# Kernel tuning notes

Hardware: AMD Instinct MI355X
Metric: run time of the kernel (lower is better)

The kernel has to match this reference:

```python
import jax, jax.numpy as jnp
import numpy as np

B, T, D_IN, P, Q, D_OUT = 128, 1024, 64, 128, 2, 64


def _lstm_layer(x, w_ih, w_hh, b):
    """One LSTM layer, batch_first. x: [B,T,Din], w_ih: [4P,Din], w_hh: [4P,P], b: [4P].
    PyTorch gate order: i, f, g, o."""
    # Precompute input contribution for all timesteps (the big, parallel GEMM).
    gx = jnp.einsum('btd,gd->btg', x, w_ih) + b          # [B,T,4P]
    gx_t = jnp.swapaxes(gx, 0, 1)                        # [T,B,4P] for scan
    p = w_hh.shape[1]
    h0 = jnp.zeros((x.shape[0], p), dtype=x.dtype)
    c0 = jnp.zeros((x.shape[0], p), dtype=x.dtype)

    def step(carry, g_in):
        h, c = carry
        g = g_in + h @ w_hh.T                            # [B,4P]
        i, f, gg, o = jnp.split(g, 4, axis=-1)
        i = jax.nn.sigmoid(i)
        f = jax.nn.sigmoid(f)
        gg = jnp.tanh(gg)
        o = jax.nn.sigmoid(o)
        c = f * c + i * gg
        h = o * jnp.tanh(c)
        return (h, c), h

    _, hs = jax.lax.scan(step, (h0, c0), gx_t)           # hs: [T,B,P]
    return jnp.swapaxes(hs, 0, 1)                        # [B,T,P]


def setup_inputs() -> dict:
    key = jax.random.key(0)
    ks = jax.random.split(key, 8)
    x = jax.random.normal(ks[0], (B, T, D_IN), dtype=jnp.float32)
    # weight_ih: kaiming-normal-ish; weight_hh: orthogonal-ish (random normal is a fine stand-in
    # numerically; init distribution doesn't change the math being tested).
    w_ih0 = jax.random.normal(ks[1], (4 * P, D_IN), dtype=jnp.float32) * (1.0 / np.sqrt(D_IN))
    w_hh0 = jax.random.normal(ks[2], (4 * P, P), dtype=jnp.float32) * (1.0 / np.sqrt(P))
    w_ih1 = jax.random.normal(ks[3], (4 * P, P), dtype=jnp.float32) * (1.0 / np.sqrt(P))
    w_hh1 = jax.random.normal(ks[4], (4 * P, P), dtype=jnp.float32) * (1.0 / np.sqrt(P))
    # biases initialized to zero in the original (bias_ih + bias_hh folded into one per layer
    # would be equivalent math; keep both for faithfulness)
    b_ih = jnp.zeros((Q, 4 * P), dtype=jnp.float32)
    b_hh = jnp.zeros((Q, 4 * P), dtype=jnp.float32)
    fc_w = jax.random.normal(ks[5], (D_OUT, P), dtype=jnp.float32) * np.sqrt(2.0 / P)
    fc_b = jnp.zeros((D_OUT,), dtype=jnp.float32)
    return {"x": x, "w_ih0": w_ih0, "w_hh0": w_hh0, "w_ih1": w_ih1, "w_hh1": w_hh1,
            "b_ih": b_ih, "b_hh": b_hh, "fc_w": fc_w, "fc_b": fc_b}


def reference(x, w_ih0, w_hh0, w_ih1, w_hh1, b_ih, b_hh, fc_w, fc_b):
    h = _lstm_layer(x, w_ih0, w_hh0, b_ih[0] + b_hh[0])   # layer 0: [B,T,P]
    h = _lstm_layer(h, w_ih1, w_hh1, b_ih[1] + b_hh[1])   # layer 1: [B,T,P]
    return jnp.einsum('btp,op->bto', h, fc_w) + fc_b      # [B,T,D_OUT]
```

## Files before the change

### kernel.cpp

```cpp
#include <hip/hip_runtime.h>

#define NT 1024
#define RINGS 256

typedef _Float16 half8 __attribute__((ext_vector_type(8)));
typedef _Float16 half4 __attribute__((ext_vector_type(4)));
typedef float f32x4 __attribute__((ext_vector_type(4)));
typedef unsigned long long u64;
struct U2 { u64 a, b; };

__device__ __forceinline__ f32x4 MFMA(half8 a, half8 b, f32x4 c) {
  return __builtin_amdgcn_mfma_f32_16x16x32_f16(a, b, c, 0, 0, 0);
}
__device__ __forceinline__ float sigf(float x) {
  return __builtin_amdgcn_rcpf(1.0f + __expf(-x));
}
__device__ __forceinline__ float tanhf2(float x) {
  float ax = fabsf(x);
  float e = __expf(-2.0f * ax);
  float t = (1.0f - e) * __builtin_amdgcn_rcpf(1.0f + e);
  return copysignf(t, x);
}
__device__ __forceinline__ half8 cvt8(float4 c0, float4 c1) {
  half8 hv;
  hv[0] = (_Float16)c0.x; hv[1] = (_Float16)c0.y;
  hv[2] = (_Float16)c0.z; hv[3] = (_Float16)c0.w;
  hv[4] = (_Float16)c1.x; hv[5] = (_Float16)c1.y;
  hv[6] = (_Float16)c1.z; hv[7] = (_Float16)c1.w;
  return hv;
}
__device__ __forceinline__ half8 ldring(const _Float16* p) {
  const u64* q = (const u64*)p;
  U2 uu;
  uu.a = __hip_atomic_load(q, __ATOMIC_RELAXED, __HIP_MEMORY_SCOPE_AGENT);
  uu.b = __hip_atomic_load(q + 1, __ATOMIC_RELAXED, __HIP_MEMORY_SCOPE_AGENT);
  return __builtin_bit_cast(half8, uu);
}
__device__ __forceinline__ unsigned wpoll(unsigned* p, unsigned tgt,
                                          unsigned cached, int l) {
  unsigned c = cached;
  while (c < tgt) {
    unsigned pv = 0;
    if (l == 0)
      pv = __hip_atomic_load(p, __ATOMIC_ACQUIRE, __HIP_MEMORY_SCOPE_AGENT);
    c = (unsigned)__builtin_amdgcn_readfirstlane((int)pv);
    if (c < tgt) __builtin_amdgcn_s_sleep(2);
  }
  return c;
}

__global__ __launch_bounds__(256) void prep_x(const float* __restrict__ x,
                                              _Float16* __restrict__ Xf) {
  int t0 = blockIdx.x * 256 + threadIdx.x;
  int l = t0 & 63;
  int fid = t0 >> 6;
  int kt = fid & 1;
  int t = (fid >> 1) & (NT - 1);
  int g = fid >> 11;
  int bt = g * 16 + (l & 15);
  int kb = kt * 32 + (l >> 4) * 4;
  const float* src = x + ((size_t)bt * NT + (size_t)t) * 64 + kb;
  float4 v0 = *(const float4*)src;
  float4 v1 = *(const float4*)(src + 16);
  *(half8*)(Xf + (size_t)fid * 512 + l * 8) = cvt8(v0, v1);
}

__global__ __launch_bounds__(512, 1) void lstm_main(
    const float* __restrict__ wih0, const float* __restrict__ whh0,
    const float* __restrict__ wih1, const float* __restrict__ whh1,
    const float* __restrict__ bih, const float* __restrict__ bhh,
    const float* __restrict__ fcw, const float* __restrict__ fcb,
    const _Float16* __restrict__ Xf, _Float16* __restrict__ ringH0,
    unsigned* __restrict__ flags, float* __restrict__ out) {
  const int tid = threadIdx.x;
  const int w = tid >> 6, l = tid & 63;
  const int n = l & 15, lg = l >> 4;
  const bool producer = blockIdx.x < 8;
  const int g = blockIdx.x & 7;

  __shared__ _Float16 hfr[2][4][64][8];
  __shared__ _Float16 fcl[4][4][64][8];

  _Float16* ringG = ringH0 + (size_t)g * RINGS * 2048;
  unsigned* prog = flags + g * 16;
  unsigned* cons = flags + (8 + g) * 16;
  const half8 hz = {0, 0, 0, 0, 0, 0, 0, 0};

  if (producer) {
    half8 A[4][6];
    f32x4 bias[4];
#pragma unroll
    for (int q = 0; q < 4; ++q) {
      int row = (w + 8 * q) * 16 + n;
#pragma unroll
      for (int kt = 0; kt < 2; ++kt) {
        const float* wp = wih0 + (size_t)row * 64 + kt * 32 + lg * 4;
        A[q][kt] = cvt8(*(const float4*)wp, *(const float4*)(wp + 16));
      }
#pragma unroll
      for (int kt = 0; kt < 4; ++kt) {
        const float* wp = whh0 + (size_t)row * 128 + kt * 32 + lg * 4;
        A[q][2 + kt] = cvt8(*(const float4*)wp, *(const float4*)(wp + 16));
      }
      int rb = (w + 8 * q) * 16 + lg * 4;
      f32x4 bv;
#pragma unroll
      for (int r = 0; r < 4; ++r) bv[r] = bih[rb + r] + bhh[rb + r];
      bias[q] = bv;
    }
    if (tid < 256) ((half8*)&hfr[1][0][0][0])[tid] = hz;
    const _Float16* XfG = Xf + (size_t)g * NT * 1024;
    half8 x0 = *(const half8*)(XfG + l * 8);
    half8 x1 = *(const half8*)(XfG + 512 + l * 8);
    f32x4 cst = {0.f, 0.f, 0.f, 0.f};
    unsigned Cc = 0;
    __syncthreads();
    for (int s = 0; s < NT; ++s) {
      half8 xn0, xn1;
      if (s + 1 < NT) {
        const _Float16* p = XfG + (size_t)(s + 1) * 1024 + l * 8;
        xn0 = *(const half8*)p;
        xn1 = *(const half8*)(p + 512);
      }
      if (s >= 224 && (s & 31) == 0)
        Cc = wpoll(cons, (unsigned)(s - 192), Cc, l);
      const int rdk = (s + 1) & 1;
      half8 b2 = *(const half8*)&hfr[rdk][0][l][0];
      half8 b3 = *(const half8*)&hfr[rdk][1][l][0];
      half8 b4 = *(const half8*)&hfr[rdk][2][l][0];
      half8 b5 = *(const half8*)&hfr[rdk][3][l][0];
      f32x4 acc0 = bias[0], acc1 = bias[1], acc2 = bias[2], acc3 = bias[3];
      acc0 = MFMA(A[0][0], x0, acc0); acc1 = MFMA(A[1][0], x0, acc1);
      acc2 = MFMA(A[2][0], x0, acc2); acc3 = MFMA(A[3][0], x0, acc3);
      acc0 = MFMA(A[0][1], x1, acc0); acc1 = MFMA(A[1][1], x1, acc1);
      acc2 = MFMA(A[2][1], x1, acc2); acc3 = MFMA(A[3][1], x1, acc3);
      acc0 = MFMA(A[0][2], b2, acc0); acc1 = MFMA(A[1][2], b2, acc1);
      acc2 = MFMA(A[2][2], b2, acc2); acc3 = MFMA(A[3][2], b2, acc3);
      acc0 = MFMA(A[0][3], b3, acc0); acc1 = MFMA(A[1][3], b3, acc1);
      acc2 = MFMA(A[2][3], b3, acc2); acc3 = MFMA(A[3][3], b3, acc3);
      acc0 = MFMA(A[0][4], b4, acc0); acc1 = MFMA(A[1][4], b4, acc1);
      acc2 = MFMA(A[2][4], b4, acc2); acc3 = MFMA(A[3][4], b4, acc3);
      acc0 = MFMA(A[0][5], b5, acc0); acc1 = MFMA(A[1][5], b5, acc1);
      acc2 = MFMA(A[2][5], b5, acc2); acc3 = MFMA(A[3][5], b5, acc3);
      half4 hh;
#pragma unroll
      for (int r = 0; r < 4; ++r) {
        float iv = sigf(acc0[r]), fv = sigf(acc1[r]);
        float gv = tanhf2(acc2[r]), ov = sigf(acc3[r]);
        cst[r] = fv * cst[r] + iv * gv;
        hh[r] = (_Float16)(ov * tanhf2(cst[r]));
      }
      *(half4*)&hfr[s & 1][w >> 1][l][(w & 1) << 2] = hh;
      {
        u64 uh = __builtin_bit_cast(u64, hh);
        __hip_atomic_store(
            (u64*)(ringG + (size_t)(s & (RINGS - 1)) * 2048 +
                   (w >> 1) * 512 + l * 8 + (w & 1) * 4),
            uh, __ATOMIC_RELAXED, __HIP_MEMORY_SCOPE_AGENT);
      }
      asm volatile("s_waitcnt lgkmcnt(0)" ::: "memory");
      __builtin_amdgcn_sched_barrier(0);
      __builtin_amdgcn_s_barrier();
      __builtin_amdgcn_sched_barrier(0);
      if ((s & 31) == 31) {
        asm volatile("s_waitcnt vmcnt(0)" ::: "memory");
        __builtin_amdgcn_sched_barrier(0);
        __builtin_amdgcn_s_barrier();
        __builtin_amdgcn_sched_barrier(0);
        if (tid == 0)
          __hip_atomic_store(prog, (unsigned)(s + 1), __ATOMIC_RELEASE,
                             __HIP_MEMORY_SCOPE_AGENT);
      }
      x0 = xn0;
      x1 = xn1;
    }
  } else {
    half8 A[4][8];
    f32x4 bias[4], fcbv = {0.f, 0.f, 0.f, 0.f};
#pragma unroll
    for (int q = 0; q < 4; ++q) {
      int row = (w + 8 * q) * 16 + n;
#pragma unroll
      for (int kt = 0; kt < 4; ++kt) {
        const float* wp = wih1 + (size_t)row * 128 + kt * 32 + lg * 4;
        A[q][kt] = cvt8(*(const float4*)wp, *(const float4*)(wp + 16));
      }
#pragma unroll
      for (int kt = 0; kt < 4; ++kt) {
        const float* wp = whh1 + (size_t)row * 128 + kt * 32 + lg * 4;
        A[q][4 + kt] = cvt8(*(const float4*)wp, *(const float4*)(wp + 16));
      }
      int rb = (w + 8 * q) * 16 + lg * 4;
      f32x4 bv;
#pragma unroll
      for (int r = 0; r < 4; ++r)
        bv[r] = bih[512 + rb + r] + bhh[512 + rb + r];
      bias[q] = bv;
    }
    if (w < 4) {
      int frow = (w << 4) + n;
#pragma unroll
      for (int kt = 0; kt < 4; ++kt) {
        const float* wp = fcw + (size_t)frow * 128 + kt * 32 + lg * 4;
        *(half8*)&fcl[w][kt][l][0] =
            cvt8(*(const float4*)wp, *(const float4*)(wp + 16));
      }
      fcbv = *(const f32x4*)(fcb + (w << 4) + lg * 4);
    }
    if (tid < 256) ((half8*)&hfr[1][0][0][0])[tid] = hz;
    float* outG = out + (size_t)((g << 4) + n) * NT * 64 + (w << 4) + lg * 4;
    f32x4 cst = {0.f, 0.f, 0.f, 0.f};
    __syncthreads();
    unsigned Pc = wpoll(prog, 2u, 0u, l);
    half8 hA0 = ldring(ringG + l * 8);
    half8 hA1 = ldring(ringG + 512 + l * 8);
    half8 hA2 = ldring(ringG + 1024 + l * 8);
    half8 hA3 = ldring(ringG + 1536 + l * 8);
    const _Float16* rb1 = ringG + 2048 + l * 8;
    half8 hB0 = ldring(rb1);
    half8 hB1 = ldring(rb1 + 512);
    half8 hB2 = ldring(rb1 + 1024);
    half8 hB3 = ldring(rb1 + 1536);

#define CSTEP(T, C0, C1, C2, C3)                                               \
  {                                                                            \
    const int rdk_ = ((T) + 1) & 1;                                            \
    half8 b4 = *(const half8*)&hfr[rdk_][0][l][0];                             \
    half8 b5 = *(const half8*)&hfr[rdk_][1][l][0];                             \
    half8 b6 = *(const half8*)&hfr[rdk_][2][l][0];                             \
    half8 b7 = *(const half8*)&hfr[rdk_][3][l][0];                             \
    f32x4 acc0 = bias[0], acc1 = bias[1], acc2 = bias[2], acc3 = bias[3];      \
    acc0 = MFMA(A[0][0], C0, acc0); acc1 = MFMA(A[1][0], C0, acc1);            \
    acc2 = MFMA(A[2][0], C0, acc2); acc3 = MFMA(A[3][0], C0, acc3);            \
    acc0 = MFMA(A[0][1], C1, acc0); acc1 = MFMA(A[1][1], C1, acc1);            \
    acc2 = MFMA(A[2][1], C1, acc2); acc3 = MFMA(A[3][1], C1, acc3);            \
    acc0 = MFMA(A[0][2], C2, acc0); acc1 = MFMA(A[1][2], C2, acc1);            \
    acc2 = MFMA(A[2][2], C2, acc2); acc3 = MFMA(A[3][2], C2, acc3);            \
    acc0 = MFMA(A[0][3], C3, acc0); acc1 = MFMA(A[1][3], C3, acc1);            \
    acc2 = MFMA(A[2][3], C3, acc2); acc3 = MFMA(A[3][3], C3, acc3);            \
    if ((T) + 2 < NT) {    \
      Pc = wpoll(prog, (unsigned)((T) + 3), Pc, l);                            \
      const _Float16* rb_ =                                                    \
          ringG + (size_t)(((T) + 2) & (RINGS - 1)) * 2048 + l * 8;            \
      C0 = ldring(rb_);        C1 = ldring(rb_ + 512);                         \
      C2 = ldring(rb_ + 1024); C3 = ldring(rb_ + 1536);                        \
    }                                                                          \
    acc0 = MFMA(A[0][4], b4, acc0); acc1 = MFMA(A[1][4], b4, acc1);            \
    acc2 = MFMA(A[2][4], b4, acc2); acc3 = MFMA(A[3][4], b4, acc3);            \
    acc0 = MFMA(A[0][5], b5, acc0); acc1 = MFMA(A[1][5], b5, acc1);            \
    acc2 = MFMA(A[2][5], b5, acc2); acc3 = MFMA(A[3][5], b5, acc3);            \
    acc0 = MFMA(A[0][6], b6, acc0); acc1 = MFMA(A[1][6], b6, acc1);            \
    acc2 = MFMA(A[2][6], b6, acc2); acc3 = MFMA(A[3][6], b6, acc3);            \
    acc0 = MFMA(A[0][7], b7, acc0); acc1 = MFMA(A[1][7], b7, acc1);            \
    acc2 = MFMA(A[2][7], b7, acc2); acc3 = MFMA(A[3][7], b7, acc3);            \
    if (w < 4) {                           \
      half8 f0 = *(const half8*)&fcl[w][0][l][0];                              \
      half8 f1 = *(const half8*)&fcl[w][1][l][0];                              \
      half8 f2 = *(const half8*)&fcl[w][2][l][0];                              \
      half8 f3 = *(const half8*)&fcl[w][3][l][0];                              \
      f32x4 afc = fcbv;                                                        \
      afc = MFMA(f0, b4, afc); afc = MFMA(f1, b5, afc);                        \
      afc = MFMA(f2, b6, afc); afc = MFMA(f3, b7, afc);                        \
      if ((T) >= 1) *(f32x4*)(outG + (size_t)((T) - 1) * 64) = afc;            \
    }                                                                          \
    half4 hh;                                                                  \
    _Pragma("unroll")                                                          \
    for (int r = 0; r < 4; ++r) {                                              \
      float iv = sigf(acc0[r]), fv = sigf(acc1[r]);                            \
      float gv = tanhf2(acc2[r]), ov = sigf(acc3[r]);                          \
      cst[r] = fv * cst[r] + iv * gv;                                          \
      hh[r] = (_Float16)(ov * tanhf2(cst[r]));                                 \
    }                                                                          \
    *(half4*)&hfr[(T) & 1][w >> 1][l][(w & 1) << 2] = hh;                      \
    if (tid == 0 && ((T) & 31) == 0)                                           \
      __hip_atomic_store(cons, (unsigned)(T), __ATOMIC_RELAXED,                \
                         __HIP_MEMORY_SCOPE_AGENT);                            \
    asm volatile("s_waitcnt lgkmcnt(0)" ::: "memory");                         \
    __builtin_amdgcn_sched_barrier(0);                                         \
    __builtin_amdgcn_s_barrier();        \
    __builtin_amdgcn_sched_barrier(0);                                         \
  }

    for (int t = 0; t < NT; t += 2) {
      CSTEP(t, hA0, hA1, hA2, hA3);
      CSTEP(t + 1, hB0, hB1, hB2, hB3);
    }
#undef CSTEP
    {
      half8 b4 = *(const half8*)&hfr[(NT + 1) & 1][0][l][0];
      half8 b5 = *(const half8*)&hfr[(NT + 1) & 1][1][l][0];
      half8 b6 = *(const half8*)&hfr[(NT + 1) & 1][2][l][0];
      half8 b7 = *(const half8*)&hfr[(NT + 1) & 1][3][l][0];
      if (w < 4) {
        half8 f0 = *(const half8*)&fcl[w][0][l][0];
        half8 f1 = *(const half8*)&fcl[w][1][l][0];
        half8 f2 = *(const half8*)&fcl[w][2][l][0];
        half8 f3 = *(const half8*)&fcl[w][3][l][0];
        f32x4 afc = fcbv;
        afc = MFMA(f0, b4, afc); afc = MFMA(f1, b5, afc);
        afc = MFMA(f2, b6, afc); afc = MFMA(f3, b7, afc);
        *(f32x4*)(outG + (size_t)(NT - 1) * 64) = afc;
      }
    }
  }
}

extern "C" void kernel_launch(void* const* d_in, const int* in_sizes, int n_in,
                              void* d_out, int out_size, void* d_ws, size_t ws_size,
                              hipStream_t stream) {
  const float* x     = (const float*)d_in[0];
  const float* w_ih0 = (const float*)d_in[1];
  const float* w_hh0 = (const float*)d_in[2];
  const float* w_ih1 = (const float*)d_in[3];
  const float* w_hh1 = (const float*)d_in[4];
  const float* b_ih  = (const float*)d_in[5];
  const float* b_hh  = (const float*)d_in[6];
  const float* fc_w  = (const float*)d_in[7];
  const float* fc_b  = (const float*)d_in[8];

  _Float16* Xf   = (_Float16*)d_ws;
  _Float16* ring = (_Float16*)((char*)d_ws + (16u << 20));
  unsigned* flags = (unsigned*)((char*)d_ws + (24u << 20));

  hipMemsetAsync(flags, 0, 4096, stream);
  prep_x<<<4096, 256, 0, stream>>>(x, Xf);
  lstm_main<<<16, 512, 0, stream>>>(w_ih0, w_hh0, w_ih1, w_hh1, b_ih, b_hh,
                                    fc_w, fc_b, Xf, ring, flags,
                                    (float*)d_out);
}
```

Baseline: 1.324 ms.

## Split LSTM into four pipelined block roles, moving input projections off recurrent path

The kernel now has 32 blocks in four roles: an x-projection producer, a layer-0 recurrence block, an h0-to-layer-1 input projection block and a layer-1 recurrence block with the FC head. They communicate through fp32 gate rings in global memory with progress flags. The recurrent blocks now run only the hidden-state MFMAs each step, which shortens the serial per-step critical path. The separate prep_x kernel is dropped and x is converted to fp16 inline. The cost is extra global-memory traffic for fp32 gate preactivations and more flag polling between blocks, and the tighter coupling raises deadlock and latency risk.

After: 1.855 ms. 40.1% more time.

```diff
diff --git a/kernel.cpp b/kernel.cpp
--- a/kernel.cpp
+++ b/kernel.cpp
@@ -1,7 +1,9 @@
 #include <hip/hip_runtime.h>
 
 #define NT 1024
-#define RINGS 256
+#define H0S 256
+#define GXS 64
+#define GYS 64
 
 typedef _Float16 half8 __attribute__((ext_vector_type(8)));
 typedef _Float16 half4 __attribute__((ext_vector_type(4)));
@@ -29,12 +31,28 @@
   hv[6] = (_Float16)c1.z; hv[7] = (_Float16)c1.w;
   return hv;
 }
-__device__ __forceinline__ half8 ldring(const _Float16* p) {
+__device__ __forceinline__ half8 ldringh(const _Float16* p) {
   const u64* q = (const u64*)p;
   U2 uu;
   uu.a = __hip_atomic_load(q, __ATOMIC_RELAXED, __HIP_MEMORY_SCOPE_AGENT);
   uu.b = __hip_atomic_load(q + 1, __ATOMIC_RELAXED, __HIP_MEMORY_SCOPE_AGENT);
   return __builtin_bit_cast(half8, uu);
+}
+__device__ __forceinline__ f32x4 ld16f(const float* p) {
+  const u64* q = (const u64*)p;
+  U2 uu;
+  uu.a = __hip_atomic_load(q, __ATOMIC_RELAXED, __HIP_MEMORY_SCOPE_AGENT);
+  uu.b = __hip_atomic_load(q + 1, __ATOMIC_RELAXED, __HIP_MEMORY_SCOPE_AGENT);
+  return __builtin_bit_cast(f32x4, uu);
+}
+__device__ __forceinline__ void st16f(float* p, f32x4 v) {
+  U2 uu = __builtin_bit_cast(U2, v);
+  __hip_atomic_store((u64*)p, uu.a, __ATOMIC_RELAXED, __HIP_MEMORY_SCOPE_AGENT);
+  __hip_atomic_store((u64*)p + 1, uu.b, __ATOMIC_RELAXED, __HIP_MEMORY_SCOPE_AGENT);
+}
+__device__ __forceinline__ void st8h(_Float16* p, half4 v) {
+  u64 uh = __builtin_bit_cast(u64, v);
+  __hip_atomic_store((u64*)p, uh, __ATOMIC_RELAXED, __HIP_MEMORY_SCOPE_AGENT);
 }
 __device__ __forceinline__ unsigned wpoll(unsigned* p, unsigned tgt,
                                           unsigned cached, int l) {
@@ -49,45 +67,35 @@
   return c;
 }
 
-__global__ __launch_bounds__(256) void prep_x(const float* __restrict__ x,
-                                              _Float16* __restrict__ Xf) {
-  int t0 = blockIdx.x * 256 + threadIdx.x;
-  int l = t0 & 63;
-  int fid = t0 >> 6;
-  int kt = fid & 1;
-  int t = (fid >> 1) & (NT - 1);
-  int g = fid >> 11;
-  int bt = g * 16 + (l & 15);
-  int kb = kt * 32 + (l >> 4) * 4;
-  const float* src = x + ((size_t)bt * NT + (size_t)t) * 64 + kb;
-  float4 v0 = *(const float4*)src;
-  float4 v1 = *(const float4*)(src + 16);
-  *(half8*)(Xf + (size_t)fid * 512 + l * 8) = cvt8(v0, v1);
-}
-
 __global__ __launch_bounds__(512, 1) void lstm_main(
+    const float* __restrict__ x,
     const float* __restrict__ wih0, const float* __restrict__ whh0,
     const float* __restrict__ wih1, const float* __restrict__ whh1,
     const float* __restrict__ bih, const float* __restrict__ bhh,
     const float* __restrict__ fcw, const float* __restrict__ fcb,
-    const _Float16* __restrict__ Xf, _Float16* __restrict__ ringH0,
-    unsigned* __restrict__ flags, float* __restrict__ out) {
+    _Float16* __restrict__ ringH0, float* __restrict__ ringGX,
+    float* __restrict__ ringGY, unsigned* __restrict__ flags,
+    float* __restrict__ out) {
   const int tid = threadIdx.x;
   const int w = tid >> 6, l = tid & 63;
   const int n = l & 15, lg = l >> 4;
-  const bool producer = blockIdx.x < 8;
+  const int role = blockIdx.x >> 3;
   const int g = blockIdx.x & 7;
 
   __shared__ _Float16 hfr[2][4][64][8];
   __shared__ _Float16 fcl[4][4][64][8];
 
-  _Float16* ringG = ringH0 + (size_t)g * RINGS * 2048;
-  unsigned* prog = flags + g * 16;
-  unsigned* cons = flags + (8 + g) * 16;
+  _Float16* h0G = ringH0 + (size_t)g * H0S * 2048;
+  float* gxG = ringGX + (size_t)g * GXS * 8192;
+  float* gyG = ringGY + (size_t)g * GYS * 8192;
+  unsigned* pX0 = flags + (0 * 8 + g) * 16;
+  unsigned* pP  = flags + (1 * 8 + g) * 16;
+  unsigned* pX1 = flags + (2 * 8 + g) * 16;
+  unsigned* cY  = flags + (3 * 8 + g) * 16;
   const half8 hz = {0, 0, 0, 0, 0, 0, 0, 0};
 
-  if (producer) {
-    half8 A[4][6];
+  if (role == 0) {
+    half8 A[4][2];
     f32x4 bias[4];
 #pragma unroll
     for (int q = 0; q < 4; ++q) {
@@ -97,86 +105,137 @@
         const float* wp = wih0 + (size_t)row * 64 + kt * 32 + lg * 4;
         A[q][kt] = cvt8(*(const float4*)wp, *(const float4*)(wp + 16));
       }
-#pragma unroll
-      for (int kt = 0; kt < 4; ++kt) {
-        const float* wp = whh0 + (size_t)row * 128 + kt * 32 + lg * 4;
-        A[q][2 + kt] = cvt8(*(const float4*)wp, *(const float4*)(wp + 16));
-      }
       int rb = (w + 8 * q) * 16 + lg * 4;
       f32x4 bv;
 #pragma unroll
       for (int r = 0; r < 4; ++r) bv[r] = bih[rb + r] + bhh[rb + r];
       bias[q] = bv;
     }
-    if (tid < 256) ((half8*)&hfr[1][0][0][0])[tid] = hz;
-    const _Float16* XfG = Xf + (size_t)g * NT * 1024;
-    half8 x0 = *(const half8*)(XfG + l * 8);
-    half8 x1 = *(const half8*)(XfG + 512 + l * 8);
-    f32x4 cst = {0.f, 0.f, 0.f, 0.f};
-    unsigned Cc = 0;
-    __syncthreads();
-    for (int s = 0; s < NT; ++s) {
-      half8 xn0, xn1;
-      if (s + 1 < NT) {
-        const _Float16* p = XfG + (size_t)(s + 1) * 1024 + l * 8;
-        xn0 = *(const half8*)p;
-        xn1 = *(const half8*)(p + 512);
-      }
-      if (s >= 224 && (s & 31) == 0)
-        Cc = wpoll(cons, (unsigned)(s - 192), Cc, l);
-      const int rdk = (s + 1) & 1;
-      half8 b2 = *(const half8*)&hfr[rdk][0][l][0];
-      half8 b3 = *(const half8*)&hfr[rdk][1][l][0];
-      half8 b4 = *(const half8*)&hfr[rdk][2][l][0];
-      half8 b5 = *(const half8*)&hfr[rdk][3][l][0];
-      f32x4 acc0 = bias[0], acc1 = bias[1], acc2 = bias[2], acc3 = bias[3];
-      acc0 = MFMA(A[0][0], x0, acc0); acc1 = MFMA(A[1][0], x0, acc1);
-      acc2 = MFMA(A[2][0], x0, acc2); acc3 = MFMA(A[3][0], x0, acc3);
-      acc0 = MFMA(A[0][1], x1, acc0); acc1 = MFMA(A[1][1], x1, acc1);
-      acc2 = MFMA(A[2][1], x1, acc2); acc3 = MFMA(A[3][1], x1, acc3);
-      acc0 = MFMA(A[0][2], b2, acc0); acc1 = MFMA(A[1][2], b2, acc1);
-      acc2 = MFMA(A[2][2], b2, acc2); acc3 = MFMA(A[3][2], b2, acc3);
-      acc0 = MFMA(A[0][3], b3, acc0); acc1 = MFMA(A[1][3], b3, acc1);
-      acc2 = MFMA(A[2][3], b3, acc2); acc3 = MFMA(A[3][3], b3, acc3);
-      acc0 = MFMA(A[0][4], b4, acc0); acc1 = MFMA(A[1][4], b4, acc1);
-      acc2 = MFMA(A[2][4], b4, acc2); acc3 = MFMA(A[3][4], b4, acc3);
-      acc0 = MFMA(A[0][5], b5, acc0); acc1 = MFMA(A[1][5], b5, acc1);
-      acc2 = MFMA(A[2][5], b5, acc2); acc3 = MFMA(A[3][5], b5, acc3);
-      half4 hh;
-#pragma unroll
-      for (int r = 0; r < 4; ++r) {
-        float iv = sigf(acc0[r]), fv = sigf(acc1[r]);
-        float gv = tanhf2(acc2[r]), ov = sigf(acc3[r]);
-        cst[r] = fv * cst[r] + iv * gv;
-        hh[r] = (_Float16)(ov * tanhf2(cst[r]));
-      }
-      *(half4*)&hfr[s & 1][w >> 1][l][(w & 1) << 2] = hh;
-      {
-        u64 uh = __builtin_bit_cast(u64, hh);
-        __hip_atomic_store(
-            (u64*)(ringG + (size_t)(s & (RINGS - 1)) * 2048 +
-                   (w >> 1) * 512 + l * 8 + (w & 1) * 4),
-            uh, __ATOMIC_RELAXED, __HIP_MEMORY_SCOPE_AGENT);
-      }
-      asm volatile("s_waitcnt lgkmcnt(0)" ::: "memory");
-      __builtin_amdgcn_sched_barrier(0);
-      __builtin_amdgcn_s_barrier();
-      __builtin_amdgcn_sched_barrier(0);
-      if ((s & 31) == 31) {
+    const float* xL = x + (size_t)(g * 16 + n) * NT * 64 + lg * 4;
+    float4 c00 = *(const float4*)(xL);
+    float4 c01 = *(const float4*)(xL + 16);
+    float4 c10 = *(const float4*)(xL + 32);
+    float4 c11 = *(const float4*)(xL + 48);
+    unsigned Pp = 0;
+    for (int u = 0; u < NT; ++u) {
+      float4 n00, n01, n10, n11;
+      if (u + 1 < NT) {
+        const float* p = xL + (size_t)(u + 1) * 64;
+        n00 = *(const float4*)(p);
+        n01 = *(const float4*)(p + 16);
+        n10 = *(const float4*)(p + 32);
+        n11 = *(const float4*)(p + 48);
+      }
+      half8 b0 = cvt8(c00, c01), b1 = cvt8(c10, c11);
+      f32x4 a0 = bias[0], a1 = bias[1], a2 = bias[2], a3 = bias[3];
+      a0 = MFMA(A[0][0], b0, a0); a1 = MFMA(A[1][0], b0, a1);
+      a2 = MFMA(A[2][0], b0, a2); a3 = MFMA(A[3][0], b0, a3);
+      a0 = MFMA(A[0][1], b1, a0); a1 = MFMA(A[1][1], b1, a1);
+      a2 = MFMA(A[2][1], b1, a2); a3 = MFMA(A[3][1], b1, a3);
+      float* gp = gxG + (size_t)(u & (GXS - 1)) * 8192;
+      st16f(gp + ((w + 0) * 64 + l) * 4, a0);
+      st16f(gp + ((w + 8) * 64 + l) * 4, a1);
+      st16f(gp + ((w + 16) * 64 + l) * 4, a2);
+      st16f(gp + ((w + 24) * 64 + l) * 4, a3);
+      if (u >= 64 && (u & 15) == 0)
+        Pp = wpoll(pP, (unsigned)(u - 48), Pp, l);
+      if ((u & 7) == 7) {
         asm volatile("s_waitcnt vmcnt(0)" ::: "memory");
         __builtin_amdgcn_sched_barrier(0);
         __builtin_amdgcn_s_barrier();
         __builtin_amdgcn_sched_barrier(0);
         if (tid == 0)
-          __hip_atomic_store(prog, (unsigned)(s + 1), __ATOMIC_RELEASE,
+          __hip_atomic_store(pX0, (unsigned)(u + 1), __ATOMIC_RELEASE,
                              __HIP_MEMORY_SCOPE_AGENT);
       }
-      x0 = xn0;
-      x1 = xn1;
-    }
-  } else {
-    half8 A[4][8];
-    f32x4 bias[4], fcbv = {0.f, 0.f, 0.f, 0.f};
+      c00 = n00; c01 = n01; c10 = n10; c11 = n11;
+    }
+  } else if (role == 1) {
+    half8 A[4][4];
+#pragma unroll
+    for (int q = 0; q < 4; ++q) {
+      int row = (w + 8 * q) * 16 + n;
+#pragma unroll
+      for (int kt = 0; kt < 4; ++kt) {
+        const float* wp = whh0 + (size_t)row * 128 + kt * 32 + lg * 4;
+        A[q][kt] = cvt8(*(const float4*)wp, *(const float4*)(wp + 16));
+      }
+    }
+    if (tid < 256) ((half8*)&hfr[1][0][0][0])[tid] = hz;
+    f32x4 cst = {0.f, 0.f, 0.f, 0.f};
+    unsigned Px = 0, X1p = 0;
+    __syncthreads();
+    Px = wpoll(pX0, 2u, 0u, l);
+    f32x4 gA0 = ld16f(gxG + ((w + 0) * 64 + l) * 4);
+    f32x4 gA1 = ld16f(gxG + ((w + 8) * 64 + l) * 4);
+    f32x4 gA2 = ld16f(gxG + ((w + 16) * 64 + l) * 4);
+    f32x4 gA3 = ld16f(gxG + ((w + 24) * 64 + l) * 4);
+    const float* g1p = gxG + 8192;
+    f32x4 gB0 = ld16f(g1p + ((w + 0) * 64 + l) * 4);
+    f32x4 gB1 = ld16f(g1p + ((w + 8) * 64 + l) * 4);
+    f32x4 gB2 = ld16f(g1p + ((w + 16) * 64 + l) * 4);
+    f32x4 gB3 = ld16f(g1p + ((w + 24) * 64 + l) * 4);
+
+#define PSTEP(T, G0, G1, G2, G3)                                               \
+  {                                                                            \
+    const int rdk_ = ((T) + 1) & 1;                                            \
+    half8 b0_ = *(const half8*)&hfr[rdk_][0][l][0];                            \
+    half8 b1_ = *(const half8*)&hfr[rdk_][1][l][0];                            \
+    half8 b2_ = *(const half8*)&hfr[rdk_][2][l][0];                            \
+    half8 b3_ = *(const half8*)&hfr[rdk_][3][l][0];                            \
+    f32x4 a0 = G0, a1 = G1, a2 = G2, a3 = G3;                                  \
+    a0 = MFMA(A[0][0], b0_, a0); a1 = MFMA(A[1][0], b0_, a1);                  \
+    a2 = MFMA(A[2][0], b0_, a2); a3 = MFMA(A[3][0], b0_, a3);                  \
+    a0 = MFMA(A[0][1], b1_, a0); a1 = MFMA(A[1][1], b1_, a1);                  \
+    a2 = MFMA(A[2][1], b1_, a2); a3 = MFMA(A[3][1], b1_, a3);                  \
+    a0 = MFMA(A[0][2], b2_, a0); a1 = MFMA(A[1][2], b2_, a1);                  \
+    a2 = MFMA(A[2][2], b2_, a2); a3 = MFMA(A[3][2], b2_, a3);                  \
+    a0 = MFMA(A[0][3], b3_, a0); a1 = MFMA(A[1][3], b3_, a1);                  \
+    a2 = MFMA(A[2][3], b3_, a2); a3 = MFMA(A[3][3], b3_, a3);                  \
+    if ((T) + 2 < NT) {   \
+      Px = wpoll(pX0, (unsigned)((T) + 3), Px, l);                             \
+      const float* gp_ = gxG + (size_t)(((T) + 2) & (GXS - 1)) * 8192;         \
+      G0 = ld16f(gp_ + ((w + 0) * 64 + l) * 4);                                \
+      G1 = ld16f(gp_ + ((w + 8) * 64 + l) * 4);                                \
+      G2 = ld16f(gp_ + ((w + 16) * 64 + l) * 4);                               \
+      G3 = ld16f(gp_ + ((w + 24) * 64 + l) * 4);                               \
+    }                                                                          \
+    half4 hh;                                                                  \
+    _Pragma("unroll")                                                          \
+    for (int r = 0; r < 4; ++r) {                                              \
+      float iv = sigf(a0[r]), fv = sigf(a1[r]);                                \
+      float gv = tanhf2(a2[r]), ov = sigf(a3[r]);                              \
+      cst[r] = fv * cst[r] + iv * gv;                                          \
+      hh[r] = (_Float16)(ov * tanhf2(cst[r]));                                 \
+    }                                                                          \
+    *(half4*)&hfr[(T) & 1][w >> 1][l][(w & 1) << 2] = hh;                      \
+    st8h(h0G + (size_t)((T) & (H0S - 1)) * 2048 + (w >> 1) * 512 + l * 8 +     \
+             (w & 1) * 4, hh);                                                 \
+    if ((T) >= 224 && ((T) & 31) == 0)     \
+      X1p = wpoll(pX1, (unsigned)((T) - 192), X1p, l);                         \
+    asm volatile("s_waitcnt lgkmcnt(0)" ::: "memory");                         \
+    __builtin_amdgcn_sched_barrier(0);                                         \
+    __builtin_amdgcn_s_barrier();              \
+    __builtin_amdgcn_sched_barrier(0);                                         \
+    if (((T) & 31) == 31) {                     \
+      asm volatile("s_waitcnt vmcnt(0)" ::: "memory");                         \
+      __builtin_amdgcn_sched_barrier(0);                                       \
+      __builtin_amdgcn_s_barrier();                                            \
+      __builtin_amdgcn_sched_barrier(0);                                       \
+      if (tid == 0)                                                            \
+        __hip_atomic_store(pP, (unsigned)((T) + 1), __ATOMIC_RELEASE,          \
+                           __HIP_MEMORY_SCOPE_AGENT);                          \
+    }                                                                          \
+  }
+
+    for (int s = 0; s < NT; s += 2) {
+      PSTEP(s, gA0, gA1, gA2, gA3);
+      PSTEP(s + 1, gB0, gB1, gB2, gB3);
+    }
+#undef PSTEP
+  } else if (role == 2) {
+    half8 A[4][4];
+    f32x4 bias[4];
 #pragma unroll
     for (int q = 0; q < 4; ++q) {
       int row = (w + 8 * q) * 16 + n;
@@ -185,17 +244,76 @@
         const float* wp = wih1 + (size_t)row * 128 + kt * 32 + lg * 4;
         A[q][kt] = cvt8(*(const float4*)wp, *(const float4*)(wp + 16));
       }
-#pragma unroll
-      for (int kt = 0; kt < 4; ++kt) {
-        const float* wp = whh1 + (size_t)row * 128 + kt * 32 + lg * 4;
-        A[q][4 + kt] = cvt8(*(const float4*)wp, *(const float4*)(wp + 16));
-      }
       int rb = (w + 8 * q) * 16 + lg * 4;
       f32x4 bv;
 #pragma unroll
       for (int r = 0; r < 4; ++r)
         bv[r] = bih[512 + rb + r] + bhh[512 + rb + r];
       bias[q] = bv;
+    }
+    unsigned Pp = wpoll(pP, 2u, 0u, l), cYp = 0;
+    half8 hA0 = ldringh(h0G + l * 8);
+    half8 hA1 = ldringh(h0G + 512 + l * 8);
+    half8 hA2 = ldringh(h0G + 1024 + l * 8);
+    half8 hA3 = ldringh(h0G + 1536 + l * 8);
+    const _Float16* h1p = h0G + 2048 + l * 8;
+    half8 hB0 = ldringh(h1p);
+    half8 hB1 = ldringh(h1p + 512);
+    half8 hB2 = ldringh(h1p + 1024);
+    half8 hB3 = ldringh(h1p + 1536);
+
+#define XSTEP(U, H0_, H1_, H2_, H3_)                                           \
+  {                                                                            \
+    f32x4 a0 = bias[0], a1 = bias[1], a2 = bias[2], a3 = bias[3];              \
+    a0 = MFMA(A[0][0], H0_, a0); a1 = MFMA(A[1][0], H0_, a1);                  \
+    a2 = MFMA(A[2][0], H0_, a2); a3 = MFMA(A[3][0], H0_, a3);                  \
+    a0 = MFMA(A[0][1], H1_, a0); a1 = MFMA(A[1][1], H1_, a1);                  \
+    a2 = MFMA(A[2][1], H1_, a2); a3 = MFMA(A[3][1], H1_, a3);                  \
+    a0 = MFMA(A[0][2], H2_, a0); a1 = MFMA(A[1][2], H2_, a1);                  \
+    a2 = MFMA(A[2][2], H2_, a2); a3 = MFMA(A[3][2], H2_, a3);                  \
+    a0 = MFMA(A[0][3], H3_, a0); a1 = MFMA(A[1][3], H3_, a1);                  \
+    a2 = MFMA(A[2][3], H3_, a2); a3 = MFMA(A[3][3], H3_, a3);                  \
+    if ((U) + 2 < NT) {                                  \
+      Pp = wpoll(pP, (unsigned)((U) + 3), Pp, l);                              \
+      const _Float16* hp_ =                                                    \
+          h0G + (size_t)(((U) + 2) & (H0S - 1)) * 2048 + l * 8;                \
+      H0_ = ldringh(hp_);        H1_ = ldringh(hp_ + 512);                     \
+      H2_ = ldringh(hp_ + 1024); H3_ = ldringh(hp_ + 1536);                    \
+    }                                                                          \
+    float* gp_ = gyG + (size_t)((U) & (GYS - 1)) * 8192;                       \
+    st16f(gp_ + ((w + 0) * 64 + l) * 4, a0);                                   \
+    st16f(gp_ + ((w + 8) * 64 + l) * 4, a1);                                   \
+    st16f(gp_ + ((w + 16) * 64 + l) * 4, a2);                                  \
+    st16f(gp_ + ((w + 24) * 64 + l) * 4, a3);                                  \
+    if ((U) >= 40 && ((U) & 7) == 0)      \
+      cYp = wpoll(cY, (unsigned)((U) - 40), cYp, l);                           \
+    if (((U) & 7) == 7) {                         \
+      asm volatile("s_waitcnt vmcnt(0)" ::: "memory");                         \
+      __builtin_amdgcn_sched_barrier(0);                                       \
+      __builtin_amdgcn_s_barrier();                                            \
+      __builtin_amdgcn_sched_barrier(0);                                       \
+      if (tid == 0)                                                            \
+        __hip_atomic_store(pX1, (unsigned)((U) + 1), __ATOMIC_RELEASE,         \
+                           __HIP_MEMORY_SCOPE_AGENT);                          \
+    }                                                                          \
+  }
+
+    for (int u = 0; u < NT; u += 2) {
+      XSTEP(u, hA0, hA1, hA2, hA3);
+      XSTEP(u + 1, hB0, hB1, hB2, hB3);
+    }
+#undef XSTEP
+  } else {
+    half8 A[4][4];
+    f32x4 fcbv = {0.f, 0.f, 0.f, 0.f};
+#pragma unroll
+    for (int q = 0; q < 4; ++q) {
+      int row = (w + 8 * q) * 16 + n;
+#pragma unroll
+      for (int kt = 0; kt < 4; ++kt) {
+        const float* wp = whh1 + (size_t)row * 128 + kt * 32 + lg * 4;
+        A[q][kt] = cvt8(*(const float4*)wp, *(const float4*)(wp + 16));
+      }
     }
     if (w < 4) {
       int frow = (w << 4) + n;
@@ -210,95 +328,89 @@
     if (tid < 256) ((half8*)&hfr[1][0][0][0])[tid] = hz;
     float* outG = out + (size_t)((g << 4) + n) * NT * 64 + (w << 4) + lg * 4;
     f32x4 cst = {0.f, 0.f, 0.f, 0.f};
+    unsigned X1p = 0;
     __syncthreads();
-    unsigned Pc = wpoll(prog, 2u, 0u, l);
-    half8 hA0 = ldring(ringG + l * 8);
-    half8 hA1 = ldring(ringG + 512 + l * 8);
-    half8 hA2 = ldring(ringG + 1024 + l * 8);
-    half8 hA3 = ldring(ringG + 1536 + l * 8);
-    const _Float16* rb1 = ringG + 2048 + l * 8;
-    half8 hB0 = ldring(rb1);
-    half8 hB1 = ldring(rb1 + 512);
-    half8 hB2 = ldring(rb1 + 1024);
-    half8 hB3 = ldring(rb1 + 1536);
-
-#define CSTEP(T, C0, C1, C2, C3)                                               \
+    X1p = wpoll(pX1, 2u, 0u, l);
+    f32x4 gA0 = ld16f(gyG + ((w + 0) * 64 + l) * 4);
+    f32x4 gA1 = ld16f(gyG + ((w + 8) * 64 + l) * 4);
+    f32x4 gA2 = ld16f(gyG + ((w + 16) * 64 + l) * 4);
+    f32x4 gA3 = ld16f(gyG + ((w + 24) * 64 + l) * 4);
+    const float* g1p = gyG + 8192;
+    f32x4 gB0 = ld16f(g1p + ((w + 0) * 64 + l) * 4);
+    f32x4 gB1 = ld16f(g1p + ((w + 8) * 64 + l) * 4);
+    f32x4 gB2 = ld16f(g1p + ((w + 16) * 64 + l) * 4);
+    f32x4 gB3 = ld16f(g1p + ((w + 24) * 64 + l) * 4);
+
+#define YSTEP(T, G0, G1, G2, G3)                                               \
   {                                                                            \
     const int rdk_ = ((T) + 1) & 1;                                            \
-    half8 b4 = *(const half8*)&hfr[rdk_][0][l][0];                             \
-    half8 b5 = *(const half8*)&hfr[rdk_][1][l][0];                             \
-    half8 b6 = *(const half8*)&hfr[rdk_][2][l][0];                             \
-    half8 b7 = *(const half8*)&hfr[rdk_][3][l][0];                             \
-    f32x4 acc0 = bias[0], acc1 = bias[1], acc2 = bias[2], acc3 = bias[3];      \
-    acc0 = MFMA(A[0][0], C0, acc0); acc1 = MFMA(A[1][0], C0, acc1);            \
-    acc2 = MFMA(A[2][0], C0, acc2); acc3 = MFMA(A[3][0], C0, acc3);            \
-    acc0 = MFMA(A[0][1], C1, acc0); acc1 = MFMA(A[1][1], C1, acc1);            \
-    acc2 = MFMA(A[2][1], C1, acc2); acc3 = MFMA(A[3][1], C1, acc3);            \
-    acc0 = MFMA(A[0][2], C2, acc0); acc1 = MFMA(A[1][2], C2, acc1);            \
-    acc2 = MFMA(A[2][2], C2, acc2); acc3 = MFMA(A[3][2], C2, acc3);            \
-    acc0 = MFMA(A[0][3], C3, acc0); acc1 = MFMA(A[1][3], C3, acc1);            \
-    acc2 = MFMA(A[2][3], C3, acc2); acc3 = MFMA(A[3][3], C3, acc3);            \
-    if ((T) + 2 < NT) {    \
-      Pc = wpoll(prog, (unsigned)((T) + 3), Pc, l);                            \
-      const _Float16* rb_ =                                                    \
-          ringG + (size_t)(((T) + 2) & (RINGS - 1)) * 2048 + l * 8;            \
-      C0 = ldring(rb_);        C1 = ldring(rb_ + 512);                         \
-      C2 = ldring(rb_ + 1024); C3 = ldring(rb_ + 1536);                        \
-    }                                                                          \
-    acc0 = MFMA(A[0][4], b4, acc0); acc1 = MFMA(A[1][4], b4, acc1);            \
-    acc2 = MFMA(A[2][4], b4, acc2); acc3 = MFMA(A[3][4], b4, acc3);            \
-    acc0 = MFMA(A[0][5], b5, acc0); acc1 = MFMA(A[1][5], b5, acc1);            \
-    acc2 = MFMA(A[2][5], b5, acc2); acc3 = MFMA(A[3][5], b5, acc3);            \
-    acc0 = MFMA(A[0][6], b6, acc0); acc1 = MFMA(A[1][6], b6, acc1);            \
-    acc2 = MFMA(A[2][6], b6, acc2); acc3 = MFMA(A[3][6], b6, acc3);            \
-    acc0 = MFMA(A[0][7], b7, acc0); acc1 = MFMA(A[1][7], b7, acc1);            \
-    acc2 = MFMA(A[2][7], b7, acc2); acc3 = MFMA(A[3][7], b7, acc3);            \
-    if (w < 4) {                           \
+    half8 b0_ = *(const half8*)&hfr[rdk_][0][l][0];                            \
+    half8 b1_ = *(const half8*)&hfr[rdk_][1][l][0];                            \
+    half8 b2_ = *(const half8*)&hfr[rdk_][2][l][0];                            \
+    half8 b3_ = *(const half8*)&hfr[rdk_][3][l][0];                            \
+    f32x4 a0 = G0, a1 = G1, a2 = G2, a3 = G3;                                  \
+    a0 = MFMA(A[0][0], b0_, a0); a1 = MFMA(A[1][0], b0_, a1);                  \
+    a2 = MFMA(A[2][0], b0_, a2); a3 = MFMA(A[3][0], b0_, a3);                  \
+    a0 = MFMA(A[0][1], b1_, a0); a1 = MFMA(A[1][1], b1_, a1);                  \
+    a2 = MFMA(A[2][1], b1_, a2); a3 = MFMA(A[3][1], b1_, a3);                  \
+    a0 = MFMA(A[0][2], b2_, a0); a1 = MFMA(A[1][2], b2_, a1);                  \
+    a2 = MFMA(A[2][2], b2_, a2); a3 = MFMA(A[3][2], b2_, a3);                  \
+    a0 = MFMA(A[0][3], b3_, a0); a1 = MFMA(A[1][3], b3_, a1);                  \
+    a2 = MFMA(A[2][3], b3_, a2); a3 = MFMA(A[3][3], b3_, a3);                  \
+    if ((T) + 2 < NT) {                                 \
+      X1p = wpoll(pX1, (unsigned)((T) + 3), X1p, l);                           \
+      const float* gp_ = gyG + (size_t)(((T) + 2) & (GYS - 1)) * 8192;         \
+      G0 = ld16f(gp_ + ((w + 0) * 64 + l) * 4);                                \
+      G1 = ld16f(gp_ + ((w + 8) * 64 + l) * 4);                                \
+      G2 = ld16f(gp_ + ((w + 16) * 64 + l) * 4);                               \
+      G3 = ld16f(gp_ + ((w + 24) * 64 + l) * 4);                               \
+    }                                                                          \
+    if (w < 4) {                                            \
       half8 f0 = *(const half8*)&fcl[w][0][l][0];                              \
       half8 f1 = *(const half8*)&fcl[w][1][l][0];                              \
       half8 f2 = *(const half8*)&fcl[w][2][l][0];                              \
       half8 f3 = *(const half8*)&fcl[w][3][l][0];                              \
       f32x4 afc = fcbv;                                                        \
-      afc = MFMA(f0, b4, afc); afc = MFMA(f1, b5, afc);                        \
-      afc = MFMA(f2, b6, afc); afc = MFMA(f3, b7, afc);                        \
+      afc = MFMA(f0, b0_, afc); afc = MFMA(f1, b1_, afc);                      \
+      afc = MFMA(f2, b2_, afc); afc = MFMA(f3, b3_, afc);                      \
       if ((T) >= 1) *(f32x4*)(outG + (size_t)((T) - 1) * 64) = afc;            \
     }                                                                          \
     half4 hh;                                                                  \
     _Pragma("unroll")                                                          \
     for (int r = 0; r < 4; ++r) {                                              \
-      float iv = sigf(acc0[r]), fv = sigf(acc1[r]);                            \
-      float gv = tanhf2(acc2[r]), ov = sigf(acc3[r]);                          \
+      float iv = sigf(a0[r]), fv = sigf(a1[r]);                                \
+      float gv = tanhf2(a2[r]), ov = sigf(a3[r]);                              \
       cst[r] = fv * cst[r] + iv * gv;                                          \
       hh[r] = (_Float16)(ov * tanhf2(cst[r]));                                 \
     }                                                                          \
     *(half4*)&hfr[(T) & 1][w >> 1][l][(w & 1) << 2] = hh;                      \
-    if (tid == 0 && ((T) & 31) == 0)                                           \
-      __hip_atomic_store(cons, (unsigned)(T), __ATOMIC_RELAXED,                \
+    if (tid == 0 && ((T) & 15) == 0) \
+      __hip_atomic_store(cY, (unsigned)(T), __ATOMIC_RELAXED,                  \
                          __HIP_MEMORY_SCOPE_AGENT);                            \
     asm volatile("s_waitcnt lgkmcnt(0)" ::: "memory");                         \
     __builtin_amdgcn_sched_barrier(0);                                         \
-    __builtin_amdgcn_s_barrier();        \
+    __builtin_amdgcn_s_barrier();             \
     __builtin_amdgcn_sched_barrier(0);                                         \
   }
 
     for (int t = 0; t < NT; t += 2) {
-      CSTEP(t, hA0, hA1, hA2, hA3);
-      CSTEP(t + 1, hB0, hB1, hB2, hB3);
-    }
-#undef CSTEP
+      YSTEP(t, gA0, gA1, gA2, gA3);
+      YSTEP(t + 1, gB0, gB1, gB2, gB3);
+    }
+#undef YSTEP
     {
-      half8 b4 = *(const half8*)&hfr[(NT + 1) & 1][0][l][0];
-      half8 b5 = *(const half8*)&hfr[(NT + 1) & 1][1][l][0];
-      half8 b6 = *(const half8*)&hfr[(NT + 1) & 1][2][l][0];
-      half8 b7 = *(const half8*)&hfr[(NT + 1) & 1][3][l][0];
+      half8 b0_ = *(const half8*)&hfr[(NT + 1) & 1][0][l][0];
+      half8 b1_ = *(const half8*)&hfr[(NT + 1) & 1][1][l][0];
+      half8 b2_ = *(const half8*)&hfr[(NT + 1) & 1][2][l][0];
+      half8 b3_ = *(const half8*)&hfr[(NT + 1) & 1][3][l][0];
       if (w < 4) {
         half8 f0 = *(const half8*)&fcl[w][0][l][0];
         half8 f1 = *(const half8*)&fcl[w][1][l][0];
         half8 f2 = *(const half8*)&fcl[w][2][l][0];
         half8 f3 = *(const half8*)&fcl[w][3][l][0];
         f32x4 afc = fcbv;
-        afc = MFMA(f0, b4, afc); afc = MFMA(f1, b5, afc);
-        afc = MFMA(f2, b6, afc); afc = MFMA(f3, b7, afc);
+        afc = MFMA(f0, b0_, afc); afc = MFMA(f1, b1_, afc);
+        afc = MFMA(f2, b2_, afc); afc = MFMA(f3, b3_, afc);
         *(f32x4*)(outG + (size_t)(NT - 1) * 64) = afc;
       }
     }
@@ -318,13 +430,13 @@
   const float* fc_w  = (const float*)d_in[7];
   const float* fc_b  = (const float*)d_in[8];
 
-  _Float16* Xf   = (_Float16*)d_ws;
-  _Float16* ring = (_Float16*)((char*)d_ws + (16u << 20));
-  unsigned* flags = (unsigned*)((char*)d_ws + (24u << 20));
+  _Float16* ringH0 = (_Float16*)d_ws;
+  float* ringGX = (float*)((char*)d_ws + (8u << 20));
+  float* ringGY = (float*)((char*)d_ws + (24u << 20));
+  unsigned* flags = (unsigned*)((char*)d_ws + (40u << 20));
 
   hipMemsetAsync(flags, 0, 4096, stream);
-  prep_x<<<4096, 256, 0, stream>>>(x, Xf);
-  lstm_main<<<16, 512, 0, stream>>>(w_ih0, w_hh0, w_ih1, w_hh1, b_ih, b_hh,
-                                    fc_w, fc_b, Xf, ring, flags,
+  lstm_main<<<32, 512, 0, stream>>>(x, w_ih0, w_hh0, w_ih1, w_hh1, b_ih, b_hh,
+                                    fc_w, fc_b, ringH0, ringGX, ringGY, flags,
                                     (float*)d_out);
 }
```
